# Optimization experiments

Hardware: AMD Instinct MI355X
Metric: run time of the kernel (lower is better)

Reference implementation:

```python
import jax, jax.numpy as jnp
import numpy as np
import math

IN_DIM = 128
OUT_DIM = 128
EDGE_DIM = 16
LN_EPS = 1e-5


def setup_inputs() -> dict:
    key = jax.random.key(0)
    ks = jax.random.split(key, 6)
    bs, N = 8, 512
    x = jax.random.normal(ks[0], (bs, N, IN_DIM), dtype=jnp.float32)
    edge_feats = jax.random.normal(ks[1], (bs, N, N, EDGE_DIM), dtype=jnp.float32)
    # fc weight (out_dim, in_dim), xavier-uniform scale
    lim_w = math.sqrt(6.0 / (IN_DIM + OUT_DIM))
    W = jax.random.uniform(ks[2], (OUT_DIM, IN_DIM), minval=-lim_w, maxval=lim_w, dtype=jnp.float32)
    # attn_fc weight (1, 2*out_dim+edge_dim) split into a_src | a_dst | a_e
    fan_in = 2 * OUT_DIM + EDGE_DIM
    lim_a = math.sqrt(6.0 / (fan_in + 1))
    a = jax.random.uniform(ks[3], (fan_in,), minval=-lim_a, maxval=lim_a, dtype=jnp.float32)
    a_src, a_dst, a_e = a[:OUT_DIM], a[OUT_DIM:2 * OUT_DIM], a[2 * OUT_DIM:]
    gamma = jnp.ones((OUT_DIM,), dtype=jnp.float32)
    beta = jnp.zeros((OUT_DIM,), dtype=jnp.float32)
    return {"x": x, "edge_feats": edge_feats, "W": W, "a_src": a_src,
            "a_dst": a_dst, "a_e": a_e, "gamma": gamma, "beta": beta}


def reference(x, edge_feats, W, a_src, a_dst, a_e, gamma, beta):
    # h: (bs, N, out_dim)
    h = jnp.einsum('bni,oi->bno', x, W)
    scale = 1.0 / math.sqrt(OUT_DIM)
    # Decomposed rank-1 attention score: attn_fc([h_i, h_j, e_ij]) =
    # h_i.a_src + h_j.a_dst + e_ij.a_e  -- identical math, no (bs,N,N,2D+E) tensor.
    s_i = jnp.einsum('bnd,d->bn', h, a_src)           # row term (index i)
    s_j = jnp.einsum('bnd,d->bn', h, a_dst)           # col term (index j)
    s_e = jnp.einsum('bije,e->bij', edge_feats, a_e)  # edge term
    e_ij = (s_i[:, :, None] + s_j[:, None, :] + s_e) * scale  # (bs, N, N)
    # max-subtract then softmax over j (jax.nn.softmax is already max-stable,
    # and softmax(e - max) == softmax(e))
    alpha = jax.nn.softmax(e_ij, axis=-1)
    # weighted sum over neighbors j (dropout skipped: eval mode)
    h_prime = jnp.einsum('bij,bjd->bid', alpha, h)
    # LayerNorm over last dim
    mu = jnp.mean(h_prime, axis=-1, keepdims=True)
    var = jnp.var(h_prime, axis=-1, keepdims=True)
    out = (h_prime - mu) * jax.lax.rsqrt(var + LN_EPS) * gamma + beta
    return out
```

## Files before the change

kernel.cpp:

```cpp
#include <hip/hip_runtime.h>
#include <math.h>

#define NB 8
#define NN 512
#define D 128
#define TIF 4
#define JC 64
#define NCK (NN / JC)
#define K1R 8
#define LN_EPS 1e-5f
#define SCALE 0.08838834764831845f

typedef float f32x4 __attribute__((ext_vector_type(4)));

__device__ __forceinline__ float dotv(f32x4 a, f32x4 b) {
    f32x4 m = a * b;
    return m.x + m.y + m.z + m.w;
}
__device__ __forceinline__ float dot4(float4 a, float4 b) {
    return a.x * b.x + a.y * b.y + a.z * b.z + a.w * b.w;
}

__global__ __launch_bounds__(256) void k1_proj(
    const float* __restrict__ x, const float* __restrict__ W,
    const float* __restrict__ a_src, const float* __restrict__ a_dst,
    float* __restrict__ h_ws, float* __restrict__ si_ws, float* __restrict__ sj_ws)
{
    __shared__ __align__(16) float4 Wl[128][32];
    __shared__ __align__(16) float4 xl[K1R][32];
    __shared__ float redk[K1R][2][2];

    const int t = threadIdx.x;
    const int row0 = blockIdx.x * K1R;

    const float4* Wg = (const float4*)W;
#pragma unroll
    for (int k = 0; k < 16; ++k) {
        const int f = t + 256 * k;
        const int o = f >> 5, q = f & 31;
        Wl[o][q ^ (o & 7)] = Wg[f];
    }
    xl[t >> 5][t & 31] = ((const float4*)(x + (size_t)row0 * D))[t];
    __syncthreads();

    const int o = t & 127;
    const int rb = (t >> 7) * (K1R / 2);
    float acc[K1R / 2] = {0.f, 0.f, 0.f, 0.f};
#pragma unroll
    for (int q = 0; q < 32; ++q) {
        const float4 wv = Wl[o][q ^ (o & 7)];
#pragma unroll
        for (int r = 0; r < K1R / 2; ++r) acc[r] += dot4(wv, xl[rb + r][q]);
    }
    const float as = a_src[o], ad = a_dst[o];
#pragma unroll
    for (int r = 0; r < K1R / 2; ++r) {
        h_ws[(size_t)(row0 + rb + r) * D + o] = acc[r];
        float vs = acc[r] * as, vd = acc[r] * ad;
#pragma unroll
        for (int m = 32; m >= 1; m >>= 1) {
            vs += __shfl_xor(vs, m);
            vd += __shfl_xor(vd, m);
        }
        if ((t & 63) == 0) {
            redk[rb + r][0][(t >> 6) & 1] = vs;
            redk[rb + r][1][(t >> 6) & 1] = vd;
        }
    }
    __syncthreads();
    if (t < K1R) si_ws[row0 + t] = redk[t][0][0] + redk[t][0][1];
    else if (t < 2 * K1R) {
        const int r = t - K1R;
        sj_ws[row0 + r] = redk[r][1][0] + redk[r][1][1];
    }
}

__global__ __launch_bounds__(256, 4) void kfused(
    const float* __restrict__ ef, const float* __restrict__ a_e,
    const float* __restrict__ gamma, const float* __restrict__ beta,
    const float* __restrict__ h_ws,
    const float* __restrict__ sj_ws, float* __restrict__ out)
{
    __shared__ float sj_l[NN];
    __shared__ __align__(16) float ab[2][JC][TIF];
    __shared__ __align__(16) float part[4][TIF][D];
    __shared__ __align__(16) float lw[4][TIF];

    const int t = threadIdx.x;
    const int w = t >> 6;
    const int lane = t & 63;
    const int bid = blockIdx.x;
    const int b = bid >> 7;
    const int i0 = (bid & 127) * TIF;

    sj_l[t] = sj_ws[b * NN + t];
    sj_l[t + 256] = sj_ws[b * NN + t + 256];

    const int c = t & 3;
    const f32x4 A = ((const f32x4*)a_e)[c];
    const f32x4* ef4 = (const f32x4*)ef + ((size_t)b * NN + i0) * NN * 4;

    const int jl = t >> 2;
    const int dl = (t & 31) << 2;
    const int g = t >> 5;
    const float* hb = h_ws + (size_t)b * NN * D;

    f32x4 acc0 = {0.f, 0.f, 0.f, 0.f};
    f32x4 acc1 = {0.f, 0.f, 0.f, 0.f};
    f32x4 acc2 = {0.f, 0.f, 0.f, 0.f};
    f32x4 acc3 = {0.f, 0.f, 0.f, 0.f};
    f32x4 lp   = {0.f, 0.f, 0.f, 0.f};

    f32x4 p0 = ef4[0 * 2048 + t];
    f32x4 p1 = ef4[1 * 2048 + t];
    f32x4 p2 = ef4[2 * 2048 + t];
    f32x4 p3 = ef4[3 * 2048 + t];

    __syncthreads();

    for (int ck = 0; ck < NCK; ++ck) {
        {
            float d0 = dotv(p0, A), d1 = dotv(p1, A);
            float d2 = dotv(p2, A), d3 = dotv(p3, A);
            d0 += __shfl_xor(d0, 1); d0 += __shfl_xor(d0, 2);
            d1 += __shfl_xor(d1, 1); d1 += __shfl_xor(d1, 2);
            d2 += __shfl_xor(d2, 1); d2 += __shfl_xor(d2, 2);
            d3 += __shfl_xor(d3, 1); d3 += __shfl_xor(d3, 2);
            const float dsel = (c == 0) ? d0 : (c == 1) ? d1 : (c == 2) ? d2 : d3;
            const float al = __expf((sj_l[ck * JC + jl] + dsel) * SCALE);
            ab[ck & 1][jl][c] = al;
        }
        if (ck + 1 < NCK) {
            const int off = (ck + 1) * 256 + t;
            p0 = ef4[0 * 2048 + off];
            p1 = ef4[1 * 2048 + off];
            p2 = ef4[2 * 2048 + off];
            p3 = ef4[3 * 2048 + off];
        }
        asm volatile("s_waitcnt lgkmcnt(0)" ::: "memory");
        __builtin_amdgcn_s_barrier();
        __builtin_amdgcn_sched_barrier(0);

        {
            const float* abp = &ab[ck & 1][0][0];
            const int jbase = ck * JC + (g << 3);
#pragma unroll
            for (int jt = 0; jt < 2; ++jt) {
                const int j0 = (g << 3) + (jt << 2);
                const int jg = ck * JC + j0;
                const f32x4 hv0 = *(const f32x4*)(hb + (size_t)(jg + 0) * D + dl);
                const f32x4 hv1 = *(const f32x4*)(hb + (size_t)(jg + 1) * D + dl);
                const f32x4 hv2 = *(const f32x4*)(hb + (size_t)(jg + 2) * D + dl);
                const f32x4 hv3 = *(const f32x4*)(hb + (size_t)(jg + 3) * D + dl);
                const f32x4 a0v = *(const f32x4*)(abp + (j0 + 0) * TIF);
                const f32x4 a1v = *(const f32x4*)(abp + (j0 + 1) * TIF);
                const f32x4 a2v = *(const f32x4*)(abp + (j0 + 2) * TIF);
                const f32x4 a3v = *(const f32x4*)(abp + (j0 + 3) * TIF);
                acc0 += hv0 * a0v.x + hv1 * a1v.x + hv2 * a2v.x + hv3 * a3v.x;
                acc1 += hv0 * a0v.y + hv1 * a1v.y + hv2 * a2v.y + hv3 * a3v.y;
                acc2 += hv0 * a0v.z + hv1 * a1v.z + hv2 * a2v.z + hv3 * a3v.z;
                acc3 += hv0 * a0v.w + hv1 * a1v.w + hv2 * a2v.w + hv3 * a3v.w;
                lp += a0v + a1v + a2v + a3v;
            }
            (void)jbase;
        }
    }

#pragma unroll
    for (int cc = 0; cc < 4; ++cc) {
        acc0[cc] += __shfl_xor(acc0[cc], 32);
        acc1[cc] += __shfl_xor(acc1[cc], 32);
        acc2[cc] += __shfl_xor(acc2[cc], 32);
        acc3[cc] += __shfl_xor(acc3[cc], 32);
        lp[cc]   += __shfl_xor(lp[cc], 32);
    }
    if (lane < 32) {
        *(f32x4*)&part[w][0][dl] = acc0;
        *(f32x4*)&part[w][1][dl] = acc1;
        *(f32x4*)&part[w][2][dl] = acc2;
        *(f32x4*)&part[w][3][dl] = acc3;
    }
    if (lane == 0) *(f32x4*)&lw[w][0] = lp;
    __syncthreads();

    {
        const float l_r = lw[0][w] + lw[1][w] + lw[2][w] + lw[3][w];
        const float inv = 1.0f / l_r;
        const int d0 = lane, d1 = lane + 64;
        float v0 = 0.f, v1 = 0.f;
#pragma unroll
        for (int pw = 0; pw < 4; ++pw) {
            v0 += part[pw][w][d0];
            v1 += part[pw][w][d1];
        }
        v0 *= inv; v1 *= inv;
        float s = v0 + v1, qq = v0 * v0 + v1 * v1;
#pragma unroll
        for (int mm = 32; mm >= 1; mm >>= 1) {
            s += __shfl_xor(s, mm);
            qq += __shfl_xor(qq, mm);
        }
        const float mu = s * (1.f / 128.f);
        const float var = qq * (1.f / 128.f) - mu * mu;
        const float rs = rsqrtf(var + LN_EPS);
        const size_t ob = ((size_t)(b * NN + i0 + w)) * D;
        out[ob + d0] = (v0 - mu) * rs * gamma[d0] + beta[d0];
        out[ob + d1] = (v1 - mu) * rs * gamma[d1] + beta[d1];
    }
}

extern "C" void kernel_launch(void* const* d_in, const int* in_sizes, int n_in,
                              void* d_out, int out_size, void* d_ws, size_t ws_size,
                              hipStream_t stream) {
    const float* x     = (const float*)d_in[0];
    const float* ef    = (const float*)d_in[1];
    const float* W     = (const float*)d_in[2];
    const float* a_src = (const float*)d_in[3];
    const float* a_dst = (const float*)d_in[4];
    const float* a_e   = (const float*)d_in[5];
    const float* gamma = (const float*)d_in[6];
    const float* beta  = (const float*)d_in[7];
    float* out = (float*)d_out;

    float* h_ws  = (float*)d_ws;
    float* si_ws = h_ws + (size_t)NB * NN * D;
    float* sj_ws = si_ws + NB * NN;

    k1_proj<<<NB * NN / K1R, 256, 0, stream>>>(x, W, a_src, a_dst, h_ws, si_ws, sj_ws);
    kfused<<<NB * NN / TIF, 256, 0, stream>>>(ef, a_e, gamma, beta,
                                              h_ws, sj_ws, out);
}
```

Measured before the change: 49.35 us.

## Process eight query rows per block with wave-per-row edge scoring

Doubles rows per block to eight and the block size to 512 threads. Each wave now owns one row: a lane reads a full 16-float edge vector, computes the edge score without cross-lane shuffles, and keeps a running softmax denominator in a register. The alpha buffer is transposed to [row][j], and each h vector loaded from global memory now feeds eight accumulators instead of four, halving h reloads per output row. The cost is more registers per thread, so occupancy may drop, and each lane's edge loads are 64-byte strided instead of fully coalesced.

```diff
diff --git a/kernel.cpp b/kernel.cpp
--- a/kernel.cpp
+++ b/kernel.cpp
@@ -4,7 +4,7 @@
 #define NB 8
 #define NN 512
 #define D 128
-#define TIF 4
+#define TIF 8
 #define JC 64
 #define NCK (NN / JC)
 #define K1R 8
@@ -75,67 +75,62 @@
     }
 }
 
-__global__ __launch_bounds__(256, 4) void kfused(
+__global__ __launch_bounds__(512, 4) void kfused(
     const float* __restrict__ ef, const float* __restrict__ a_e,
     const float* __restrict__ gamma, const float* __restrict__ beta,
     const float* __restrict__ h_ws,
     const float* __restrict__ sj_ws, float* __restrict__ out)
 {
     __shared__ float sj_l[NN];
-    __shared__ __align__(16) float ab[2][JC][TIF];
-    __shared__ __align__(16) float part[4][TIF][D];
-    __shared__ __align__(16) float lw[4][TIF];
+    __shared__ __align__(16) float ab[2][TIF][JC];
+    __shared__ __align__(16) float part[8][TIF][D];
 
     const int t = threadIdx.x;
     const int w = t >> 6;
     const int lane = t & 63;
     const int bid = blockIdx.x;
-    const int b = bid >> 7;
-    const int i0 = (bid & 127) * TIF;
+    const int b = bid >> 6;
+    const int i0 = (bid & 63) * TIF;
 
     sj_l[t] = sj_ws[b * NN + t];
-    sj_l[t + 256] = sj_ws[b * NN + t + 256];
-
-    const int c = t & 3;
-    const f32x4 A = ((const f32x4*)a_e)[c];
-    const f32x4* ef4 = (const f32x4*)ef + ((size_t)b * NN + i0) * NN * 4;
-
-    const int jl = t >> 2;
+
+    const f32x4* ae4 = (const f32x4*)a_e;
+    const f32x4 A0 = ae4[0], A1 = ae4[1], A2 = ae4[2], A3 = ae4[3];
+
+    const f32x4* efw = (const f32x4*)ef + ((size_t)b * NN + i0 + w) * NN * 4
+                     + (size_t)lane * 4;
+
     const int dl = (t & 31) << 2;
     const int g = t >> 5;
     const float* hb = h_ws + (size_t)b * NN * D;
 
-    f32x4 acc0 = {0.f, 0.f, 0.f, 0.f};
-    f32x4 acc1 = {0.f, 0.f, 0.f, 0.f};
-    f32x4 acc2 = {0.f, 0.f, 0.f, 0.f};
-    f32x4 acc3 = {0.f, 0.f, 0.f, 0.f};
-    f32x4 lp   = {0.f, 0.f, 0.f, 0.f};
-
-    f32x4 p0 = ef4[0 * 2048 + t];
-    f32x4 p1 = ef4[1 * 2048 + t];
-    f32x4 p2 = ef4[2 * 2048 + t];
-    f32x4 p3 = ef4[3 * 2048 + t];
+    f32x4 acc0 = {0.f, 0.f, 0.f, 0.f}, acc1 = {0.f, 0.f, 0.f, 0.f};
+    f32x4 acc2 = {0.f, 0.f, 0.f, 0.f}, acc3 = {0.f, 0.f, 0.f, 0.f};
+    f32x4 acc4 = {0.f, 0.f, 0.f, 0.f}, acc5 = {0.f, 0.f, 0.f, 0.f};
+    f32x4 acc6 = {0.f, 0.f, 0.f, 0.f}, acc7 = {0.f, 0.f, 0.f, 0.f};
+    float l_reg = 0.f;
+
+    f32x4 p0 = efw[0];
+    f32x4 p1 = efw[1];
+    f32x4 p2 = efw[2];
+    f32x4 p3 = efw[3];
 
     __syncthreads();
 
     for (int ck = 0; ck < NCK; ++ck) {
         {
-            float d0 = dotv(p0, A), d1 = dotv(p1, A);
-            float d2 = dotv(p2, A), d3 = dotv(p3, A);
-            d0 += __shfl_xor(d0, 1); d0 += __shfl_xor(d0, 2);
-            d1 += __shfl_xor(d1, 1); d1 += __shfl_xor(d1, 2);
-            d2 += __shfl_xor(d2, 1); d2 += __shfl_xor(d2, 2);
-            d3 += __shfl_xor(d3, 1); d3 += __shfl_xor(d3, 2);
-            const float dsel = (c == 0) ? d0 : (c == 1) ? d1 : (c == 2) ? d2 : d3;
-            const float al = __expf((sj_l[ck * JC + jl] + dsel) * SCALE);
-            ab[ck & 1][jl][c] = al;
+            const float dsum = dotv(p0, A0) + dotv(p1, A1)
+                             + dotv(p2, A2) + dotv(p3, A3);
+            const float al = __expf((sj_l[ck * JC + lane] + dsum) * SCALE);
+            ab[ck & 1][w][lane] = al;
+            l_reg += al;
         }
         if (ck + 1 < NCK) {
-            const int off = (ck + 1) * 256 + t;
-            p0 = ef4[0 * 2048 + off];
-            p1 = ef4[1 * 2048 + off];
-            p2 = ef4[2 * 2048 + off];
-            p3 = ef4[3 * 2048 + off];
+            const f32x4* pn = efw + (ck + 1) * 256;
+            p0 = pn[0];
+            p1 = pn[1];
+            p2 = pn[2];
+            p3 = pn[3];
         }
         asm volatile("s_waitcnt lgkmcnt(0)" ::: "memory");
         __builtin_amdgcn_s_barrier();
@@ -143,26 +138,28 @@
 
         {
             const float* abp = &ab[ck & 1][0][0];
-            const int jbase = ck * JC + (g << 3);
-#pragma unroll
-            for (int jt = 0; jt < 2; ++jt) {
-                const int j0 = (g << 3) + (jt << 2);
-                const int jg = ck * JC + j0;
-                const f32x4 hv0 = *(const f32x4*)(hb + (size_t)(jg + 0) * D + dl);
-                const f32x4 hv1 = *(const f32x4*)(hb + (size_t)(jg + 1) * D + dl);
-                const f32x4 hv2 = *(const f32x4*)(hb + (size_t)(jg + 2) * D + dl);
-                const f32x4 hv3 = *(const f32x4*)(hb + (size_t)(jg + 3) * D + dl);
-                const f32x4 a0v = *(const f32x4*)(abp + (j0 + 0) * TIF);
-                const f32x4 a1v = *(const f32x4*)(abp + (j0 + 1) * TIF);
-                const f32x4 a2v = *(const f32x4*)(abp + (j0 + 2) * TIF);
-                const f32x4 a3v = *(const f32x4*)(abp + (j0 + 3) * TIF);
-                acc0 += hv0 * a0v.x + hv1 * a1v.x + hv2 * a2v.x + hv3 * a3v.x;
-                acc1 += hv0 * a0v.y + hv1 * a1v.y + hv2 * a2v.y + hv3 * a3v.y;
-                acc2 += hv0 * a0v.z + hv1 * a1v.z + hv2 * a2v.z + hv3 * a3v.z;
-                acc3 += hv0 * a0v.w + hv1 * a1v.w + hv2 * a2v.w + hv3 * a3v.w;
-                lp += a0v + a1v + a2v + a3v;
-            }
-            (void)jbase;
+            const int j0 = g << 2;
+            const int jg = ck * JC + j0;
+            const f32x4 hv0 = *(const f32x4*)(hb + (size_t)(jg + 0) * D + dl);
+            const f32x4 hv1 = *(const f32x4*)(hb + (size_t)(jg + 1) * D + dl);
+            const f32x4 hv2 = *(const f32x4*)(hb + (size_t)(jg + 2) * D + dl);
+            const f32x4 hv3 = *(const f32x4*)(hb + (size_t)(jg + 3) * D + dl);
+            const f32x4 a0v = *(const f32x4*)(abp + 0 * JC + j0);
+            const f32x4 a1v = *(const f32x4*)(abp + 1 * JC + j0);
+            const f32x4 a2v = *(const f32x4*)(abp + 2 * JC + j0);
+            const f32x4 a3v = *(const f32x4*)(abp + 3 * JC + j0);
+            const f32x4 a4v = *(const f32x4*)(abp + 4 * JC + j0);
+            const f32x4 a5v = *(const f32x4*)(abp + 5 * JC + j0);
+            const f32x4 a6v = *(const f32x4*)(abp + 6 * JC + j0);
+            const f32x4 a7v = *(const f32x4*)(abp + 7 * JC + j0);
+            acc0 += hv0 * a0v.x + hv1 * a0v.y + hv2 * a0v.z + hv3 * a0v.w;
+            acc1 += hv0 * a1v.x + hv1 * a1v.y + hv2 * a1v.z + hv3 * a1v.w;
+            acc2 += hv0 * a2v.x + hv1 * a2v.y + hv2 * a2v.z + hv3 * a2v.w;
+            acc3 += hv0 * a3v.x + hv1 * a3v.y + hv2 * a3v.z + hv3 * a3v.w;
+            acc4 += hv0 * a4v.x + hv1 * a4v.y + hv2 * a4v.z + hv3 * a4v.w;
+            acc5 += hv0 * a5v.x + hv1 * a5v.y + hv2 * a5v.z + hv3 * a5v.w;
+            acc6 += hv0 * a6v.x + hv1 * a6v.y + hv2 * a6v.z + hv3 * a6v.w;
+            acc7 += hv0 * a7v.x + hv1 * a7v.y + hv2 * a7v.z + hv3 * a7v.w;
         }
     }
 
@@ -172,24 +169,31 @@
         acc1[cc] += __shfl_xor(acc1[cc], 32);
         acc2[cc] += __shfl_xor(acc2[cc], 32);
         acc3[cc] += __shfl_xor(acc3[cc], 32);
-        lp[cc]   += __shfl_xor(lp[cc], 32);
+        acc4[cc] += __shfl_xor(acc4[cc], 32);
+        acc5[cc] += __shfl_xor(acc5[cc], 32);
+        acc6[cc] += __shfl_xor(acc6[cc], 32);
+        acc7[cc] += __shfl_xor(acc7[cc], 32);
     }
     if (lane < 32) {
         *(f32x4*)&part[w][0][dl] = acc0;
         *(f32x4*)&part[w][1][dl] = acc1;
         *(f32x4*)&part[w][2][dl] = acc2;
         *(f32x4*)&part[w][3][dl] = acc3;
-    }
-    if (lane == 0) *(f32x4*)&lw[w][0] = lp;
+        *(f32x4*)&part[w][4][dl] = acc4;
+        *(f32x4*)&part[w][5][dl] = acc5;
+        *(f32x4*)&part[w][6][dl] = acc6;
+        *(f32x4*)&part[w][7][dl] = acc7;
+    }
+#pragma unroll
+    for (int mm = 32; mm >= 1; mm >>= 1) l_reg += __shfl_xor(l_reg, mm);
     __syncthreads();
 
     {
-        const float l_r = lw[0][w] + lw[1][w] + lw[2][w] + lw[3][w];
-        const float inv = 1.0f / l_r;
+        const float inv = 1.0f / l_reg;
         const int d0 = lane, d1 = lane + 64;
         float v0 = 0.f, v1 = 0.f;
 #pragma unroll
-        for (int pw = 0; pw < 4; ++pw) {
+        for (int pw = 0; pw < 8; ++pw) {
             v0 += part[pw][w][d0];
             v1 += part[pw][w][d1];
         }
@@ -227,6 +231,6 @@
     float* sj_ws = si_ws + NB * NN;
 
     k1_proj<<<NB * NN / K1R, 256, 0, stream>>>(x, W, a_src, a_dst, h_ws, si_ws, sj_ws);
-    kfused<<<NB * NN / TIF, 256, 0, stream>>>(ef, a_e, gamma, beta,
+    kfused<<<NB * NN / TIF, 512, 0, stream>>>(ef, a_e, gamma, beta,
                                               h_ws, sj_ws, out);
 }
```

Measured after the change: 55.46 us. 1.12x slower.
